# Kernel optimization log

Hardware: AMD Instinct MI355X
Metric: run time of the kernel (lower is better)

## Reference

```python
import jax, jax.numpy as jnp
import numpy as np

PATCH = 256
N = 50000
HC = 256  # height // PATCH
WC = 256  # width // PATCH

def _gauss_kernel():
    # GaussianSmoothing(channels=1, kernel_size=3, sigma=0.5)
    g = np.exp(-(((np.arange(3, dtype=np.float64) - 1.0) / 0.5) ** 2) / 2.0) / (0.5 * np.sqrt(2 * np.pi))
    k = np.outer(g, g)
    k = k / k.sum()
    return jnp.asarray(k, jnp.float32).reshape(1, 1, 3, 3)

def setup_inputs() -> dict:
    key = jax.random.key(0)
    ks = jax.random.split(key, 12)
    h = jax.random.normal(ks[0], (N, 1024), jnp.float32)
    # unique grid cells per patch (row-major), scaled back to pixel coords
    idx = jnp.arange(N, dtype=jnp.int64 if jax.config.jax_enable_x64 else jnp.int32)
    gx = idx % WC
    gy = idx // WC
    coords = jnp.stack([gx * PATCH, gy * PATCH], axis=1)
    eps = jax.random.normal(ks[1], (1, 1, HC, WC), jnp.float32)
    s = 0.02
    W1 = jax.random.normal(ks[2], (512, 1024), jnp.float32) * s
    b1 = jnp.zeros((512,), jnp.float32)
    W2a = jax.random.normal(ks[3], (256, 512), jnp.float32) * s
    b2a = jnp.zeros((256,), jnp.float32)
    W2b = jax.random.normal(ks[4], (256, 512), jnp.float32) * s
    b2b = jnp.zeros((256,), jnp.float32)
    W3 = jax.random.normal(ks[5], (2, 256), jnp.float32) * s
    b3 = jnp.zeros((2,), jnp.float32)
    Wc = jax.random.normal(ks[6], (2, 512), jnp.float32) * s
    bc = jnp.zeros((2,), jnp.float32)
    kernel = _gauss_kernel()
    return {"h": h, "coords": coords, "eps": eps,
            "W1": W1, "b1": b1, "W2a": W2a, "b2a": b2a, "W2b": W2b, "b2b": b2b,
            "W3": W3, "b3": b3, "Wc": Wc, "bc": bc, "kernel": kernel,
            "height": 65536, "width": 65536, "slide_label": 1}

def reference(h, coords, eps, W1, b1, W2a, b2a, W2b, b2b, W3, b3, Wc, bc, kernel, height, width, slide_label):
    hc, wc = height // PATCH, width // PATCH
    x = jax.nn.relu(h @ W1.T + b1)                      # [N,512] (dropout = eval identity)
    fa = jax.nn.sigmoid(x @ W2a.T + b2a)                # [N,256]
    fb = jnp.tanh(x @ W2b.T + b2b)                      # [N,256]
    params = (fa * fb) @ W3.T + b3                      # [N,2] -> (mu, logvar) per patch
    gx = coords[:, 0] // PATCH
    gy = coords[:, 1] // PATCH
    mu = jnp.zeros((1, hc, wc), x.dtype).at[0, gy, gx].set(params[:, 0])
    logvar = jnp.zeros((1, hc, wc), x.dtype).at[0, gy, gx].set(params[:, 1])
    prior_mu = jnp.array([-5.0, 0.0], x.dtype)[slide_label]
    prior_lv = jnp.array([-1.0, 3.0], x.dtype)[slide_label]
    kl_div = (prior_lv - logvar) / 2.0 + (logvar ** 2 + (prior_mu - mu) ** 2) / (2.0 * prior_lv ** 2) - 0.5
    mu_pad = jnp.pad(mu, ((0, 0), (1, 1), (1, 1)))[None]          # [1,1,hc+2,wc+2]
    mu_sm = jax.lax.conv_general_dilated(mu_pad, kernel, (1, 1), 'VALID')  # [1,1,hc,wc]
    samples = mu_sm + eps * jnp.exp(0.5 * logvar)                  # reparameterize, broadcast to [1,1,hc,wc]
    A = jax.nn.sigmoid(samples[0])                                 # [1,hc,wc]
    patch_A = A[0, gy, gx][None]                                   # gather -> [1,N]
    M = (patch_A @ x) / patch_A.sum()                              # [1,512]
    logits = M @ Wc.T + bc                                         # [1,n_classes]
    y_probs = jax.nn.softmax(logits, axis=1)
    top_idx = jax.lax.top_k(y_probs[:, 1], 1)[1]                   # top_k=1
    top_instance = logits[top_idx]                                 # [1,n_classes]
    Y_hat = jnp.argmax(top_instance, axis=1, keepdims=True)
    Y_prob = jax.nn.softmax(top_instance, axis=1)
    return (top_instance, Y_prob, Y_hat, kl_div, y_probs, patch_A)
```

## Files before the change

kernel.cpp:

```cpp
#include <hip/hip_runtime.h>
#include <hip/hip_bf16.h>
#include <cstdint>
#include <cstddef>

#define NPATCH 50000
#define GC 256

typedef __bf16 bf16x8 __attribute__((ext_vector_type(8)));
typedef float  f32x4  __attribute__((ext_vector_type(4)));
typedef float  f32x8  __attribute__((ext_vector_type(8)));

static constexpr size_t XB_OFF    = 0;
static constexpr size_t XB_BYTES  = (size_t)50048 * 512 * 2;
static constexpr size_t W1B_OFF   = XB_OFF + XB_BYTES;
static constexpr size_t W1B_BYTES = (size_t)512 * 1024 * 2;
static constexpr size_t W2AB_OFF  = W1B_OFF + W1B_BYTES;
static constexpr size_t W2X_BYTES = (size_t)256 * 512 * 2;
static constexpr size_t W2BB_OFF  = W2AB_OFF + W2X_BYTES;
static constexpr size_t MUG_OFF   = W2BB_OFF + W2X_BYTES;
static constexpr size_t LVG_OFF   = MUG_OFF + (size_t)65536 * 4;
static constexpr size_t AG_OFF    = LVG_OFF + (size_t)65536 * 4;
static constexpr size_t MPART_OFF = AG_OFF + (size_t)65536 * 4;
static constexpr size_t SUMA_OFF  = MPART_OFF + (size_t)512 * 4;
static constexpr size_t ZERO_BYTES = SUMA_OFF + 4 - MUG_OFF;

__device__ __forceinline__ unsigned short f2bf(float f) {
  union { float f; uint32_t u; } v; v.f = f;
  uint32_t u = v.u;
  uint32_t r = (u + 0x7FFFu + ((u >> 16) & 1u)) >> 16;
  return (unsigned short)r;
}
__device__ __forceinline__ float bf2f(uint32_t bits16) {
  union { uint32_t u; float f; } v; v.u = bits16 << 16; return v.f;
}
__device__ __forceinline__ unsigned short cvt_bf16(float f) {
  __bf16 b = (__bf16)f;
  return __builtin_bit_cast(unsigned short, b);
}
__device__ __forceinline__ void gld16(const void* g, void* l) {
  __builtin_amdgcn_global_load_lds(
      (const __attribute__((address_space(1))) void*)g,
      (__attribute__((address_space(3))) void*)l, 16, 0, 0);
}
__device__ __forceinline__ bf16x8 cvt8(const float4& f0, const float4& f1) {
  f32x8 fv;
  fv[0]=f0.x; fv[1]=f0.y; fv[2]=f0.z; fv[3]=f0.w;
  fv[4]=f1.x; fv[5]=f1.y; fv[6]=f1.z; fv[7]=f1.w;
  return __builtin_convertvector(fv, bf16x8);
}

__global__ void convert_weights(const float* __restrict__ W1,
                                const float* __restrict__ W2a,
                                const float* __restrict__ W2b,
                                unsigned short* __restrict__ W1b,
                                unsigned short* __restrict__ W2ab,
                                unsigned short* __restrict__ W2bb) {
  int i = blockIdx.x * 256 + threadIdx.x;
  if (i < 512 * 1024) W1b[i] = f2bf(W1[i]);
  if (i < 256 * 512) { W2ab[i] = f2bf(W2a[i]); W2bb[i] = f2bf(W2b[i]); }
}

__global__ __launch_bounds__(512, 2) void gemm1(
    const float* __restrict__ h, const unsigned short* __restrict__ W1b,
    const float* __restrict__ b1, unsigned short* __restrict__ xb) {
  __shared__ __align__(16) unsigned short lds[40960];
  unsigned short* const A0 = lds;
  unsigned short* const A1 = lds + 8192;
  unsigned short* const B0 = lds + 16384;
  unsigned short* const B1 = lds + 24576;
  unsigned short* const B2 = lds + 32768;

  const int t  = threadIdx.x;
  const int l  = t & 63;
  const int w  = t >> 6;
  const int wm = w >> 2;
  const int wn = w & 3;
  const int g  = l >> 4;
  const int lr = l & 15;

  const int i   = blockIdx.x;
  const int xcd = i & 7;
  const int pos = i >> 3;
  const int v   = xcd * 49 + pos;
  const int rt  = v >> 1;
  const int ct  = v & 1;
  const int rowBase = rt * 256;
  const int colBase = ct * 256;

  const int tr = t >> 1;
  const int hh = t & 1;
  int gr = rowBase + tr; if (gr >= NPATCH) gr = NPATCH - 1;
  const float* ah = h + (size_t)gr * 1024 + hh * 16;
  const int sw  = (tr >> 1) & 3;
  const int aw0 = tr * 32 + ((hh * 2)     ^ sw) * 8;
  const int aw1 = tr * 32 + ((hh * 2 + 1) ^ sw) * 8;

  const int bj = (t & 3) ^ ((t >> 3) & 3);
  const unsigned short* bh  = W1b + (size_t)(colBase + (t >> 2)) * 1024 + bj * 8;
  const unsigned short* bh2 = bh + (size_t)128 * 1024;
  const int bd0 = t * 8;
  const int bd1 = 4096 + t * 8;

  const int rs = (g ^ ((lr >> 1) & 3)) * 8;
  const int abase = (wm * 128 + lr) * 32 + rs;
  const int bbase = (wn * 64 + lr) * 32 + rs;

  f32x4 acc[8][4];
#pragma unroll
  for (int m = 0; m < 8; ++m)
#pragma unroll
    for (int n = 0; n < 4; ++n) acc[m][n] = (f32x4){0.f, 0.f, 0.f, 0.f};

  unsigned short *pAr = A0, *pAw = A1;
  unsigned short *pBr = B0, *pBr1 = B1, *pBw = B2;

  float4 q0, q1, q2, q3;
  {
    gld16(bh, pBr + bd0); gld16(bh2, pBr + bd1);
    float4 f0 = *(const float4*)(ah + 0);
    float4 f1 = *(const float4*)(ah + 4);
    float4 f2 = *(const float4*)(ah + 8);
    float4 f3 = *(const float4*)(ah + 12);
    *(bf16x8*)(pAr + aw0) = cvt8(f0, f1);
    *(bf16x8*)(pAr + aw1) = cvt8(f2, f3);
    q0 = *(const float4*)(ah + 32);
    q1 = *(const float4*)(ah + 36);
    q2 = *(const float4*)(ah + 40);
    q3 = *(const float4*)(ah + 44);
    gld16(bh + 32, pBr1 + bd0); gld16(bh2 + 32, pBr1 + bd1);
  }
  asm volatile("s_waitcnt lgkmcnt(0)\n\ts_barrier" ::: "memory");

  for (int kt = 0; kt < 32; ++kt) {
    const int ka = ((kt + 2 <= 31) ? (kt + 2) : 31) * 32;
    bf16x8 af[4], bf[4];
#pragma unroll
    for (int m = 0; m < 4; ++m)
      af[m] = *(const bf16x8*)(pAr + abase + m * 512);
#pragma unroll
    for (int n = 0; n < 4; ++n)
      bf[n] = *(const bf16x8*)(pBr + bbase + n * 512);
    *(bf16x8*)(pAw + aw0) = cvt8(q0, q1);
    *(bf16x8*)(pAw + aw1) = cvt8(q2, q3);
    q0 = *(const float4*)(ah + ka + 0);
    q1 = *(const float4*)(ah + ka + 4);
    q2 = *(const float4*)(ah + ka + 8);
    q3 = *(const float4*)(ah + ka + 12);
    __builtin_amdgcn_sched_barrier(0);
    __builtin_amdgcn_s_barrier();
    __builtin_amdgcn_s_setprio(1);
#pragma unroll
    for (int m = 0; m < 4; ++m)
#pragma unroll
      for (int n = 0; n < 4; ++n)
        acc[m][n] = __builtin_amdgcn_mfma_f32_16x16x32_bf16(af[m], bf[n], acc[m][n], 0, 0, 0);
    __builtin_amdgcn_s_setprio(0);
    __builtin_amdgcn_s_barrier();
#pragma unroll
    for (int m = 0; m < 4; ++m)
      af[m] = *(const bf16x8*)(pAr + abase + (m + 4) * 512);
    gld16(bh + ka, pBw + bd0);
    gld16(bh2 + ka, pBw + bd1);
    __builtin_amdgcn_sched_barrier(0);
    __builtin_amdgcn_s_barrier();
    __builtin_amdgcn_s_setprio(1);
#pragma unroll
    for (int m = 0; m < 4; ++m)
#pragma unroll
      for (int n = 0; n < 4; ++n)
        acc[m + 4][n] = __builtin_amdgcn_mfma_f32_16x16x32_bf16(af[m], bf[n], acc[m + 4][n], 0, 0, 0);
    __builtin_amdgcn_s_setprio(0);
    asm volatile("s_waitcnt vmcnt(6) lgkmcnt(0)\n\ts_barrier" ::: "memory");
    unsigned short* tA = pAr; pAr = pAw; pAw = tA;
    unsigned short* tB = pBr; pBr = pBr1; pBr1 = pBw; pBw = tB;
  }
  asm volatile("s_waitcnt vmcnt(0) lgkmcnt(0)" ::: "memory");

  float b1v[4];
#pragma unroll
  for (int n = 0; n < 4; ++n) b1v[n] = b1[colBase + wn * 64 + n * 16 + lr];
#pragma unroll
  for (int m = 0; m < 8; ++m) {
    const int rb0 = rowBase + wm * 128 + m * 16 + g * 4;
#pragma unroll
    for (int r = 0; r < 4; ++r) {
      const int row = rb0 + r;
      if (row < NPATCH) {
        unsigned short* xrow = xb + (size_t)row * 512 + colBase + wn * 64;
#pragma unroll
        for (int n = 0; n < 4; ++n) {
          float vv = acc[m][n][r] + b1v[n];
          vv = vv > 0.f ? vv : 0.f;
          xrow[n * 16 + lr] = cvt_bf16(vv);
        }
      }
    }
  }
}

__global__ __launch_bounds__(256, 2) void gemm2(
    const unsigned short* __restrict__ xb,
    const unsigned short* __restrict__ W2ab, const unsigned short* __restrict__ W2bb,
    const float* __restrict__ b2a, const float* __restrict__ b2b,
    const float* __restrict__ W3, const float* __restrict__ b3,
    const int* __restrict__ coords,
    float* __restrict__ mug, float* __restrict__ lvg) {
  __shared__ __align__(16) unsigned short xs[64 * 40];
  __shared__ __align__(16) unsigned short was[256 * 40];
  __shared__ __align__(16) unsigned short wbs[256 * 40];
  __shared__ float pmu_s[4][64];
  __shared__ float plv_s[4][64];

  const int t = threadIdx.x;
  const int l = t & 63;
  const int w = t >> 6;
  const int g = l >> 4, lr = l & 15;
  const int rowBase = blockIdx.x * 64;

  f32x4 aa[4][4], ab[4][4];
#pragma unroll
  for (int m = 0; m < 4; ++m)
#pragma unroll
    for (int n = 0; n < 4; ++n) {
      aa[m][n] = (f32x4){0.f, 0.f, 0.f, 0.f};
      ab[m][n] = (f32x4){0.f, 0.f, 0.f, 0.f};
    }

  const int xrow = t >> 2;
  const int xc0  = (t & 3) * 8;
  const int grow = rowBase + xrow;
  const bool xval = grow < NPATCH;

  for (int kt = 0; kt < 16; ++kt) {
    const int k0 = kt * 32;
    __syncthreads();
    if (xval) {
      *(int4*)&xs[xrow * 40 + xc0] = *(const int4*)(xb + (size_t)grow * 512 + k0 + xc0);
    } else {
      int4 z = {0, 0, 0, 0};
      *(int4*)&xs[xrow * 40 + xc0] = z;
    }
#pragma unroll
    for (int j = 0; j < 4; ++j) {
      int rrow = (t >> 2) + 64 * j;
      *(int4*)&was[rrow * 40 + xc0] = *(const int4*)(W2ab + (size_t)rrow * 512 + k0 + xc0);
      *(int4*)&wbs[rrow * 40 + xc0] = *(const int4*)(W2bb + (size_t)rrow * 512 + k0 + xc0);
    }
    __syncthreads();

    bf16x8 af[4], ba[4], bb[4];
#pragma unroll
    for (int m = 0; m < 4; ++m)
      af[m] = *(const bf16x8*)&xs[(m * 16 + lr) * 40 + g * 8];
#pragma unroll
    for (int n = 0; n < 4; ++n) {
      int brow = w * 64 + n * 16 + lr;
      ba[n] = *(const bf16x8*)&was[brow * 40 + g * 8];
      bb[n] = *(const bf16x8*)&wbs[brow * 40 + g * 8];
    }
#pragma unroll
    for (int m = 0; m < 4; ++m)
#pragma unroll
      for (int n = 0; n < 4; ++n) {
        aa[m][n] = __builtin_amdgcn_mfma_f32_16x16x32_bf16(af[m], ba[n], aa[m][n], 0, 0, 0);
        ab[m][n] = __builtin_amdgcn_mfma_f32_16x16x32_bf16(af[m], bb[n], ab[m][n], 0, 0, 0);
      }
  }

  float b2av[4], b2bv[4], w30v[4], w31v[4];
#pragma unroll
  for (int n = 0; n < 4; ++n) {
    int col = w * 64 + n * 16 + lr;
    b2av[n] = b2a[col]; b2bv[n] = b2b[col];
    w30v[n] = W3[col];  w31v[n] = W3[256 + col];
  }
#pragma unroll
  for (int m = 0; m < 4; ++m) {
#pragma unroll
    for (int r = 0; r < 4; ++r) {
      float pm = 0.f, pl = 0.f;
#pragma unroll
      for (int n = 0; n < 4; ++n) {
        float a = 1.f / (1.f + __expf(-(aa[m][n][r] + b2av[n])));
        float b = tanhf(ab[m][n][r] + b2bv[n]);
        float p = a * b;
        pm += p * w30v[n];
        pl += p * w31v[n];
      }
#pragma unroll
      for (int d = 1; d < 16; d <<= 1) {
        pm += __shfl_xor(pm, d, 64);
        pl += __shfl_xor(pl, d, 64);
      }
      if (lr == 0) {
        pmu_s[w][m * 16 + g * 4 + r] = pm;
        plv_s[w][m * 16 + g * 4 + r] = pl;
      }
    }
  }
  __syncthreads();
  if (t < 64) {
    float mu = pmu_s[0][t] + pmu_s[1][t] + pmu_s[2][t] + pmu_s[3][t] + b3[0];
    float lv = plv_s[0][t] + plv_s[1][t] + plv_s[2][t] + plv_s[3][t] + b3[1];
    int row = rowBase + t;
    if (row < NPATCH) {
      int gx = coords[2 * row] >> 8;
      int gy = coords[2 * row + 1] >> 8;
      int cell = gy * GC + gx;
      mug[cell] = mu;
      lvg[cell] = lv;
    }
  }
}

__global__ void grid_ops(const float* __restrict__ mug, const float* __restrict__ lvg,
                         const float* __restrict__ eps, const float* __restrict__ kern,
                         const int* __restrict__ slide, float* __restrict__ Ag,
                         float* __restrict__ out_kl) {
  int cell = blockIdx.x * 256 + threadIdx.x;
  int iy = cell >> 8, ix = cell & 255;
  float mu = mug[cell], lv = lvg[cell];
  int sl = slide[0];
  float pm  = (sl == 0) ? -5.0f : 0.0f;
  float plv = (sl == 0) ? -1.0f : 3.0f;
  float d = pm - mu;
  out_kl[cell] = (plv - lv) * 0.5f + (lv * lv + d * d) / (2.0f * plv * plv) - 0.5f;
  float s = 0.f;
#pragma unroll
  for (int dy = 0; dy < 3; ++dy) {
#pragma unroll
    for (int dx = 0; dx < 3; ++dx) {
      int y = iy + dy - 1, x = ix + dx - 1;
      if (y >= 0 && y < GC && x >= 0 && x < GC)
        s += mug[y * GC + x] * kern[dy * 3 + dx];
    }
  }
  float sample = s + eps[cell] * __expf(0.5f * lv);
  Ag[cell] = 1.f / (1.f + __expf(-sample));
}

__global__ __launch_bounds__(256) void patch_pass(
    const float* __restrict__ Ag, const int* __restrict__ coords,
    const unsigned short* __restrict__ xb, float* __restrict__ out_pA,
    float* __restrict__ Mpart, float* __restrict__ sumA) {
  __shared__ float als[256];
  __shared__ float swave[4];
  const int t = threadIdx.x;
  const int base = blockIdx.x * 256;
  const int row = base + t;
  float a = 0.f;
  if (row < NPATCH) {
    int gx = coords[2 * row] >> 8;
    int gy = coords[2 * row + 1] >> 8;
    a = Ag[gy * GC + gx];
    out_pA[row] = a;
  }
  als[t] = a;
  float sa = a;
#pragma unroll
  for (int d = 1; d < 64; d <<= 1) sa += __shfl_xor(sa, d, 64);
  if ((t & 63) == 0) swave[t >> 6] = sa;
  __syncthreads();
  if (t == 0) atomicAdd(sumA, swave[0] + swave[1] + swave[2] + swave[3]);

  const int nrows = min(256, NPATCH - base);
  float m0 = 0.f, m1 = 0.f;
  for (int r = 0; r < nrows; ++r) {
    float av = als[r];
    const uint32_t* p = (const uint32_t*)(xb + (size_t)(base + r) * 512);
    uint32_t v = p[t];
    m0 += av * bf2f(v & 0xFFFFu);
    m1 += av * bf2f(v >> 16);
  }
  atomicAdd(&Mpart[t * 2 + 0], m0);
  atomicAdd(&Mpart[t * 2 + 1], m1);
}

__global__ void finalize(const float* __restrict__ Mpart, const float* __restrict__ sumA,
                         const float* __restrict__ Wc, const float* __restrict__ bc,
                         float* __restrict__ out) {
  const int t = threadIdx.x;
  float s = sumA[0];
  float l0 = 0.f, l1 = 0.f;
#pragma unroll
  for (int j = 0; j < 8; ++j) {
    int c = t * 8 + j;
    float m = Mpart[c] / s;
    l0 += m * Wc[c];
    l1 += m * Wc[512 + c];
  }
#pragma unroll
  for (int d = 1; d < 64; d <<= 1) {
    l0 += __shfl_xor(l0, d, 64);
    l1 += __shfl_xor(l1, d, 64);
  }
  if (t == 0) {
    l0 += bc[0]; l1 += bc[1];
    float mx = fmaxf(l0, l1);
    float e0 = __expf(l0 - mx), e1 = __expf(l1 - mx);
    float inv = 1.f / (e0 + e1);
    float p0 = e0 * inv, p1 = e1 * inv;
    out[0] = l0; out[1] = l1;
    out[2] = p0; out[3] = p1;
    out[4] = (l1 > l0) ? 1.0f : 0.0f;
    out[65541] = p0; out[65542] = p1;
  }
}

extern "C" void kernel_launch(void* const* d_in, const int* in_sizes, int n_in,
                              void* d_out, int out_size, void* d_ws, size_t ws_size,
                              hipStream_t stream) {
  const float* h      = (const float*)d_in[0];
  const int*   coords = (const int*)d_in[1];
  const float* eps    = (const float*)d_in[2];
  const float* W1     = (const float*)d_in[3];
  const float* b1     = (const float*)d_in[4];
  const float* W2a    = (const float*)d_in[5];
  const float* b2a    = (const float*)d_in[6];
  const float* W2b    = (const float*)d_in[7];
  const float* b2b    = (const float*)d_in[8];
  const float* W3     = (const float*)d_in[9];
  const float* b3     = (const float*)d_in[10];
  const float* Wc     = (const float*)d_in[11];
  const float* bc     = (const float*)d_in[12];
  const float* kern   = (const float*)d_in[13];
  const int*   slide  = (const int*)d_in[16];
  float* out = (float*)d_out;
  char*  ws  = (char*)d_ws;

  unsigned short* xb   = (unsigned short*)(ws + XB_OFF);
  unsigned short* W1b  = (unsigned short*)(ws + W1B_OFF);
  unsigned short* W2ab = (unsigned short*)(ws + W2AB_OFF);
  unsigned short* W2bb = (unsigned short*)(ws + W2BB_OFF);
  float* mug   = (float*)(ws + MUG_OFF);
  float* lvg   = (float*)(ws + LVG_OFF);
  float* Ag    = (float*)(ws + AG_OFF);
  float* Mpart = (float*)(ws + MPART_OFF);
  float* sumA  = (float*)(ws + SUMA_OFF);

  hipMemsetAsync(ws + MUG_OFF, 0, ZERO_BYTES, stream);

  convert_weights<<<2048, 256, 0, stream>>>(W1, W2a, W2b, W1b, W2ab, W2bb);
  gemm1<<<392, 512, 0, stream>>>(h, W1b, b1, xb);
  gemm2<<<782, 256, 0, stream>>>(xb, W2ab, W2bb, b2a, b2b, W3, b3, coords, mug, lvg);
  grid_ops<<<256, 256, 0, stream>>>(mug, lvg, eps, kern, slide, Ag, out + 5);
  patch_pass<<<196, 256, 0, stream>>>(Ag, coords, xb, out + 65543, Mpart, sumA);
  finalize<<<1, 64, 0, stream>>>(Mpart, sumA, Wc, bc, out);
}
```

Measured before the change: 190.9 us.

## Double-buffer gemm2 with direct global-to-LDS loads and larger 128-row tiles

Restructures gemm2 to use 512-thread blocks covering 128 rows, so each W2a/W2b tile loaded into LDS is reused across twice as many rows. Shared tiles are now double-buffered and filled with direct global-to-LDS loads (gld16) while the current tile is consumed, with one barrier per step instead of two. The padded layout is replaced by an XOR-swizzled one to avoid bank conflicts. The cost is more LDS per block and likely lower occupancy. The x-row guard is also dropped: the last block reads past row 50000 into xb's padding (sized for 50048 rows), which stays in bounds but fits the 128-row tiling only loosely.

```diff
diff --git a/kernel.cpp b/kernel.cpp
--- a/kernel.cpp
+++ b/kernel.cpp
@@ -198,24 +198,38 @@
   }
 }
 
-__global__ __launch_bounds__(256, 2) void gemm2(
+__global__ __launch_bounds__(512) void gemm2(
     const unsigned short* __restrict__ xb,
     const unsigned short* __restrict__ W2ab, const unsigned short* __restrict__ W2bb,
     const float* __restrict__ b2a, const float* __restrict__ b2b,
     const float* __restrict__ W3, const float* __restrict__ b3,
     const int* __restrict__ coords,
     float* __restrict__ mug, float* __restrict__ lvg) {
-  __shared__ __align__(16) unsigned short xs[64 * 40];
-  __shared__ __align__(16) unsigned short was[256 * 40];
-  __shared__ __align__(16) unsigned short wbs[256 * 40];
-  __shared__ float pmu_s[4][64];
-  __shared__ float plv_s[4][64];
-
-  const int t = threadIdx.x;
-  const int l = t & 63;
-  const int w = t >> 6;
-  const int g = l >> 4, lr = l & 15;
-  const int rowBase = blockIdx.x * 64;
+  __shared__ __align__(16) unsigned short xs[2][128 * 32];
+  __shared__ __align__(16) unsigned short was[2][256 * 32];
+  __shared__ __align__(16) unsigned short wbs[2][256 * 32];
+  __shared__ float pmu_s[4][128];
+  __shared__ float plv_s[4][128];
+
+  const int t  = threadIdx.x;
+  const int l  = t & 63;
+  const int w  = t >> 6;
+  const int wm = w >> 2;
+  const int wn = w & 3;
+  const int g  = l >> 4;
+  const int lr = l & 15;
+  const int rowBase = blockIdx.x * 128;
+
+  const int bj = (t & 3) ^ ((t >> 3) & 3);
+  const unsigned short* xsrc   = xb   + (size_t)(rowBase + (t >> 2)) * 512 + bj * 8;
+  const unsigned short* wasrc0 = W2ab + (size_t)(t >> 2) * 512 + bj * 8;
+  const unsigned short* wasrc1 = wasrc0 + (size_t)128 * 512;
+  const unsigned short* wbsrc0 = W2bb + (size_t)(t >> 2) * 512 + bj * 8;
+  const unsigned short* wbsrc1 = wbsrc0 + (size_t)128 * 512;
+  const int d0 = t * 8;
+  const int d1 = 4096 + t * 8;
+
+  const int rslot = (g ^ ((lr >> 1) & 3)) * 8;
 
   f32x4 aa[4][4], ab[4][4];
 #pragma unroll
@@ -226,37 +240,34 @@
       ab[m][n] = (f32x4){0.f, 0.f, 0.f, 0.f};
     }
 
-  const int xrow = t >> 2;
-  const int xc0  = (t & 3) * 8;
-  const int grow = rowBase + xrow;
-  const bool xval = grow < NPATCH;
-
+  {
+    gld16(xsrc,   &xs[0][d0]);
+    gld16(wasrc0, &was[0][d0]);
+    gld16(wasrc1, &was[0][d1]);
+    gld16(wbsrc0, &wbs[0][d0]);
+    gld16(wbsrc1, &wbs[0][d1]);
+  }
+  __syncthreads();
+
+  int cur = 0;
   for (int kt = 0; kt < 16; ++kt) {
-    const int k0 = kt * 32;
-    __syncthreads();
-    if (xval) {
-      *(int4*)&xs[xrow * 40 + xc0] = *(const int4*)(xb + (size_t)grow * 512 + k0 + xc0);
-    } else {
-      int4 z = {0, 0, 0, 0};
-      *(int4*)&xs[xrow * 40 + xc0] = z;
-    }
-#pragma unroll
-    for (int j = 0; j < 4; ++j) {
-      int rrow = (t >> 2) + 64 * j;
-      *(int4*)&was[rrow * 40 + xc0] = *(const int4*)(W2ab + (size_t)rrow * 512 + k0 + xc0);
-      *(int4*)&wbs[rrow * 40 + xc0] = *(const int4*)(W2bb + (size_t)rrow * 512 + k0 + xc0);
-    }
-    __syncthreads();
-
+    if (kt < 15) {
+      const int k0 = (kt + 1) * 32;
+      gld16(xsrc + k0,   &xs[cur ^ 1][d0]);
+      gld16(wasrc0 + k0, &was[cur ^ 1][d0]);
+      gld16(wasrc1 + k0, &was[cur ^ 1][d1]);
+      gld16(wbsrc0 + k0, &wbs[cur ^ 1][d0]);
+      gld16(wbsrc1 + k0, &wbs[cur ^ 1][d1]);
+    }
     bf16x8 af[4], ba[4], bb[4];
 #pragma unroll
     for (int m = 0; m < 4; ++m)
-      af[m] = *(const bf16x8*)&xs[(m * 16 + lr) * 40 + g * 8];
+      af[m] = *(const bf16x8*)&xs[cur][(wm * 64 + m * 16 + lr) * 32 + rslot];
 #pragma unroll
     for (int n = 0; n < 4; ++n) {
-      int brow = w * 64 + n * 16 + lr;
-      ba[n] = *(const bf16x8*)&was[brow * 40 + g * 8];
-      bb[n] = *(const bf16x8*)&wbs[brow * 40 + g * 8];
+      const int brow = (wn * 64 + n * 16 + lr) * 32 + rslot;
+      ba[n] = *(const bf16x8*)&was[cur][brow];
+      bb[n] = *(const bf16x8*)&wbs[cur][brow];
     }
 #pragma unroll
     for (int m = 0; m < 4; ++m)
@@ -265,12 +276,14 @@
         aa[m][n] = __builtin_amdgcn_mfma_f32_16x16x32_bf16(af[m], ba[n], aa[m][n], 0, 0, 0);
         ab[m][n] = __builtin_amdgcn_mfma_f32_16x16x32_bf16(af[m], bb[n], ab[m][n], 0, 0, 0);
       }
+    __syncthreads();
+    cur ^= 1;
   }
 
   float b2av[4], b2bv[4], w30v[4], w31v[4];
 #pragma unroll
   for (int n = 0; n < 4; ++n) {
-    int col = w * 64 + n * 16 + lr;
+    const int col = wn * 64 + n * 16 + lr;
     b2av[n] = b2a[col]; b2bv[n] = b2b[col];
     w30v[n] = W3[col];  w31v[n] = W3[256 + col];
   }
@@ -293,13 +306,13 @@
         pl += __shfl_xor(pl, d, 64);
       }
       if (lr == 0) {
-        pmu_s[w][m * 16 + g * 4 + r] = pm;
-        plv_s[w][m * 16 + g * 4 + r] = pl;
+        pmu_s[wn][wm * 64 + m * 16 + g * 4 + r] = pm;
+        plv_s[wn][wm * 64 + m * 16 + g * 4 + r] = pl;
       }
     }
   }
   __syncthreads();
-  if (t < 64) {
+  if (t < 128) {
     float mu = pmu_s[0][t] + pmu_s[1][t] + pmu_s[2][t] + pmu_s[3][t] + b3[0];
     float lv = plv_s[0][t] + plv_s[1][t] + plv_s[2][t] + plv_s[3][t] + b3[1];
     int row = rowBase + t;
@@ -442,7 +455,7 @@
 
   convert_weights<<<2048, 256, 0, stream>>>(W1, W2a, W2b, W1b, W2ab, W2bb);
   gemm1<<<392, 512, 0, stream>>>(h, W1b, b1, xb);
-  gemm2<<<782, 256, 0, stream>>>(xb, W2ab, W2bb, b2a, b2b, W3, b3, coords, mug, lvg);
+  gemm2<<<391, 512, 0, stream>>>(xb, W2ab, W2bb, b2a, b2b, W3, b3, coords, mug, lvg);
   grid_ops<<<256, 256, 0, stream>>>(mug, lvg, eps, kern, slide, Ag, out + 5);
   patch_pass<<<196, 256, 0, stream>>>(Ag, coords, xb, out + 65543, Mpart, sumA);
   finalize<<<1, 64, 0, stream>>>(Mpart, sumA, Wc, bc, out);
```

Result: no change. 189.1 us (-0.9%).
